# Kernel tuning notes

Measured on AMD Instinct MI355X. Metric: run time of the kernel, lower is better.

Reference implementation:

```python
import jax, jax.numpy as jnp
import numpy as np

B, S = 512, 200            # batch, max_seq_len
D = H = 512                # embedding_dim must equal hidden_dim (ht init from embedded input)
VOCAB, USERS, SKILLS, OUT = 2002, 10000, 1001, 1001


def setup_inputs() -> dict:
    key = jax.random.key(0)
    ks = jax.random.split(key, 15)
    s = 0.05
    enc_emb = jax.random.normal(ks[0], (VOCAB, D)) * s
    enc_emb = enc_emb.at[0].set(0.0)  # padding_idx=0
    P = jax.random.normal(ks[1], (USERS, H)) * s
    Q = jax.random.normal(ks[2], (SKILLS, H)) * s
    P_bias = jax.random.normal(ks[3], (USERS, 1)) * s
    Q_bias = jax.random.normal(ks[4], (SKILLS, 1)) * s
    W_ih = jax.random.normal(ks[5], (4 * H, D)) * s   # torch LSTMCell weight_ih
    W_hh = jax.random.normal(ks[6], (4 * H, H)) * s   # torch LSTMCell weight_hh
    b_ih = jax.random.normal(ks[7], (4 * H,)) * s
    b_hh = jax.random.normal(ks[8], (4 * H,)) * s
    dec_W = jax.random.normal(ks[9], (OUT, H)) * s    # nn.Linear weight
    dec_b = jax.random.normal(ks[10], (OUT,)) * s
    main_input = jax.random.randint(ks[11], (B, S), 0, VOCAB)
    target_id = jax.random.randint(ks[12], (B, 1), 0, OUT)
    user_id_sequence = jax.random.randint(ks[13], (B, S), 0, USERS)
    skill_id_sequence = jax.random.randint(ks[14], (B, S), 0, SKILLS)
    return dict(main_input=main_input, target_id=target_id,
                user_id_sequence=user_id_sequence, skill_id_sequence=skill_id_sequence,
                enc_emb=enc_emb, P=P, Q=Q, P_bias=P_bias, Q_bias=Q_bias,
                W_ih=W_ih, W_hh=W_hh, b_ih=b_ih, b_hh=b_hh, dec_W=dec_W, dec_b=dec_b)


def reference(main_input, target_id, user_id_sequence, skill_id_sequence,
              enc_emb, P, Q, P_bias, Q_bias, W_ih, W_hh, b_ih, b_hh, dec_W, dec_b):
    x = enc_emb[main_input]                                    # [B,S,D] (dropout in eval mode = identity)
    # MF extended input: sigmoid(sum(P*Q, dim=2, keepdim) + P_bias + Q_bias) -> [B,S,1]
    mf = jax.nn.sigmoid(jnp.sum(P[user_id_sequence] * Q[skill_id_sequence], axis=2, keepdims=True)
                        + P_bias[user_id_sequence] + Q_bias[skill_id_sequence])

    def step(carry, inp):
        ht, ct = carry
        xt, et = inp                                           # xt:[B,D], et:[B,1]
        ct = ct + ct * et                                      # custom gating before cell update
        gates = xt @ W_ih.T + b_ih + ht @ W_hh.T + b_hh        # [B,4H], torch gate order i,f,g,o
        i, f, g, o = jnp.split(gates, 4, axis=-1)
        ct = jax.nn.sigmoid(f) * ct + jax.nn.sigmoid(i) * jnp.tanh(g)
        ht = jax.nn.sigmoid(o) * jnp.tanh(ct)
        return (ht, ct), None

    h0 = jnp.zeros((x.shape[0], H), x.dtype)
    (ht, _), _ = jax.lax.scan(step, (h0, h0),
                              (jnp.swapaxes(x, 0, 1), jnp.swapaxes(mf, 0, 1)))
    out = ht @ dec_W.T + dec_b                                 # [B,OUT]
    out = jnp.take_along_axis(out, target_id, axis=-1)         # [B,1]
    return jax.nn.sigmoid(out)
```

## Files before the change

### kernel.cpp

```cpp
#include <hip/hip_runtime.h>

typedef __attribute__((ext_vector_type(8))) short short8;
typedef __attribute__((ext_vector_type(4))) float floatx4;
typedef unsigned int uint;
typedef unsigned short ushort;
typedef unsigned long long ull;

#define B_ 512
#define S_ 200
#define H_ 512
#define VOCAB_ 2002

__device__ __forceinline__ ushort f2bfbits(float f) {
  union { float f; uint u; } c; c.f = f;
  uint u = c.u;
  u += 0x7fffu + ((u >> 16) & 1u);
  return (ushort)(u >> 16);
}
__device__ __forceinline__ float bf2f_(ushort u) {
  union { uint i; float f; } c; c.i = ((uint)u) << 16; return c.f;
}
__device__ __forceinline__ float sigmoidf_(float x) { return 1.f / (1.f + __expf(-x)); }
__device__ __forceinline__ float tanhf_(float x) { return 2.f / (1.f + __expf(-2.f * x)) - 1.f; }
__device__ __forceinline__ float clamp30(float x) { return fminf(fmaxf(x, -30.f), 30.f); }

__device__ __forceinline__ void split8(const float* p, short8& hi, short8& lo) {
#pragma unroll
  for (int j = 0; j < 8; ++j) {
    const float f = p[j];
    const ushort h = f2bfbits(f);
    hi[j] = (short)h;
    lo[j] = (short)f2bfbits(f - bf2f_(h));
  }
}

template <typename ET>
__global__ void encg_kernel(const float* __restrict__ emb, const float* __restrict__ Wih,
                            ET* __restrict__ encg) {
  const int w = threadIdx.x >> 6, l = threadIdx.x & 63;
  const int ln = l & 15, lk = l >> 4;
  const int n = (blockIdx.x * 4 + w) * 16 + ln;
  const int m = blockIdx.y * 16 + ln;
  const int mA = (m < VOCAB_) ? m : 0;
  const float* ap = emb + (size_t)mA * 512 + lk * 8;
  const float* bp = Wih + (size_t)n * 512 + lk * 8;
  floatx4 acc = {0.f, 0.f, 0.f, 0.f};
#pragma unroll 4
  for (int kk = 0; kk < 16; ++kk) {
    short8 ah, al, bh, bl;
    split8(ap + kk * 32, ah, al);
    split8(bp + kk * 32, bh, bl);
    acc = __builtin_amdgcn_mfma_f32_16x16x32_bf16(ah, bh, acc, 0, 0, 0);
    acc = __builtin_amdgcn_mfma_f32_16x16x32_bf16(ah, bl, acc, 0, 0, 0);
    acc = __builtin_amdgcn_mfma_f32_16x16x32_bf16(al, bh, acc, 0, 0, 0);
  }
#pragma unroll
  for (int r = 0; r < 4; ++r) {
    const int mo = blockIdx.y * 16 + lk * 4 + r;
    if (mo < VOCAB_) {
      if constexpr (sizeof(ET) == 2)
        encg[(size_t)mo * 2048 + n] = (ET)f2bfbits(acc[r]);
      else
        encg[(size_t)mo * 2048 + n] = acc[r];
    }
  }
}

__global__ void mf_kernel(const int* __restrict__ us, const int* __restrict__ ss,
                          const float* __restrict__ P, const float* __restrict__ Q,
                          const float* __restrict__ Pb, const float* __restrict__ Qb,
                          float* __restrict__ etb) {
  const int s = blockIdx.x;
  const int w = threadIdx.x >> 6, l = threadIdx.x & 63;
  const int b = blockIdx.y * 4 + w;
  const int u = us[b * S_ + s];
  const int k = ss[b * S_ + s];
  const float4 p0 = *(const float4*)(P + (size_t)u * 512 + l * 8);
  const float4 p1 = *(const float4*)(P + (size_t)u * 512 + l * 8 + 4);
  const float4 q0 = *(const float4*)(Q + (size_t)k * 512 + l * 8);
  const float4 q1 = *(const float4*)(Q + (size_t)k * 512 + l * 8 + 4);
  float dot = p0.x*q0.x + p0.y*q0.y + p0.z*q0.z + p0.w*q0.w
            + p1.x*q1.x + p1.y*q1.y + p1.z*q1.z + p1.w*q1.w;
#pragma unroll
  for (int off = 32; off > 0; off >>= 1) dot += __shfl_xor(dot, off);
  if (l == 0)
    etb[s * B_ + b] = sigmoidf_(dot + Pb[u] + Qb[k]);
}

template <typename ET>
__global__ __launch_bounds__(512, 2) void lstm_kernel(
    const int* __restrict__ tok, const ET* __restrict__ encg,
    const float* __restrict__ etb, const float* __restrict__ Whh,
    const float* __restrict__ bih, const float* __restrict__ bhh,
    ushort* ht_hi, ushort* ht_lo, int* ctr) {
  __shared__ __align__(16) ushort Ah_lds[32 * 528];
  __shared__ __align__(16) ushort Al_lds[32 * 528];
  __shared__ __align__(16) float gp_lds[128 * 36];

  const int bid = blockIdx.x;
  const int g = bid & 15, ns = bid >> 4;
  const int b0 = g * 32, h0 = ns * 32;
  const int tid = threadIdx.x;
  const int w = tid >> 6, l = tid & 63;
  const int ln = l & 15, lk = l >> 4;
  const int q = w >> 1;
  const int c0 = (w & 1) * 16;

  int* const myslot = ctr + g * 256 + ns * 16;
  int* const gslots = ctr + g * 256;

  short8 Bh[16], Bl[16];
  {
    const float* wr = Whh + (size_t)(q * 512 + h0 + c0 + ln) * 512 + lk * 8;
#pragma unroll 4
    for (int kk = 0; kk < 16; ++kk)
      split8(wr + kk * 32, Bh[kk], Bl[kk]);
  }

  const int sr = tid >> 4;
  const int sc = tid & 15;
  const int hh = sc * 2;
  const int bg = b0 + sr;
  float ct0 = 0.f, ct1 = 0.f;

  float bs[4][2];
#pragma unroll
  for (int qq = 0; qq < 4; ++qq) {
    const int col = qq * 512 + h0 + hh;
    bs[qq][0] = bih[col] + bhh[col];
    bs[qq][1] = bih[col + 1] + bhh[col + 1];
  }

  for (int s = 0; s < S_; ++s) {
    const int tv = tok[bg * S_ + s];
    float ev = etb[s * B_ + bg];
    float ex[4], ey[4];
#pragma unroll
    for (int qq = 0; qq < 4; ++qq) {
      if constexpr (sizeof(ET) == 2) {
        const uint e2 = *(const uint*)((const ushort*)encg + (size_t)tv * 2048 + qq * 512 + h0 + hh);
        ex[qq] = bf2f_((ushort)(e2 & 0xffffu)); ey[qq] = bf2f_((ushort)(e2 >> 16));
      } else {
        const float2 e = *(const float2*)((const float*)encg + (size_t)tv * 2048 + qq * 512 + h0 + hh);
        ex[qq] = e.x; ey[qq] = e.y;
      }
    }

    if (s > 0) {
      if (tid < 16) {
        while (__hip_atomic_load(gslots + tid * 16, __ATOMIC_RELAXED,
                                 __HIP_MEMORY_SCOPE_AGENT) < s) {}
      }
      __syncthreads();
    }
    const size_t rdo = (size_t)(s & 1) * (B_ * H_);
    const size_t wro = (size_t)((s & 1) ^ 1) * (B_ * H_);

    {
      const size_t go = rdo + (size_t)(b0 + sr) * 512 + sc * 32;
      const int lo_ = sr * 528 + sc * 32;
#pragma unroll
      for (int i = 0; i < 8; ++i)
        *(ull*)(Ah_lds + lo_ + i * 4) =
            __hip_atomic_load((const ull*)(ht_hi + go + i * 4), __ATOMIC_RELAXED, __HIP_MEMORY_SCOPE_AGENT);
#pragma unroll
      for (int i = 0; i < 8; ++i)
        *(ull*)(Al_lds + lo_ + i * 4) =
            __hip_atomic_load((const ull*)(ht_lo + go + i * 4), __ATOMIC_RELAXED, __HIP_MEMORY_SCOPE_AGENT);
    }
    __syncthreads();

    floatx4 acc[2];
    acc[0] = (floatx4){0.f, 0.f, 0.f, 0.f};
    acc[1] = (floatx4){0.f, 0.f, 0.f, 0.f};
#pragma unroll
    for (int mt = 0; mt < 2; ++mt)
#pragma unroll
      for (int kk = 0; kk < 16; ++kk) {
        const int ao = (mt * 16 + ln) * 528 + kk * 32 + lk * 8;
        const short8 ah = *(const short8*)(Ah_lds + ao);
        const short8 al = *(const short8*)(Al_lds + ao);
        acc[mt] = __builtin_amdgcn_mfma_f32_16x16x32_bf16(ah, Bh[kk], acc[mt], 0, 0, 0);
        acc[mt] = __builtin_amdgcn_mfma_f32_16x16x32_bf16(ah, Bl[kk], acc[mt], 0, 0, 0);
        acc[mt] = __builtin_amdgcn_mfma_f32_16x16x32_bf16(al, Bh[kk], acc[mt], 0, 0, 0);
      }
#pragma unroll
    for (int mt = 0; mt < 2; ++mt)
      *(floatx4*)(gp_lds + (w * 16 + ln) * 36 + mt * 16 + lk * 4) = acc[mt];
    __syncthreads();

    {
      ev = fminf(fmaxf(ev, 0.f), 1.f);
      float Gv[4][2];
#pragma unroll
      for (int qq = 0; qq < 4; ++qq) {
        Gv[qq][0] = clamp30(gp_lds[(qq * 32 + hh) * 36 + sr] + ex[qq] + bs[qq][0]);
        Gv[qq][1] = clamp30(gp_lds[(qq * 32 + hh + 1) * 36 + sr] + ey[qq] + bs[qq][1]);
      }
      const float scale = 1.f + ev;
      float c0v = ct0 * scale;
      c0v = sigmoidf_(Gv[1][0]) * c0v + sigmoidf_(Gv[0][0]) * tanhf_(Gv[2][0]);
      const float h0v = sigmoidf_(Gv[3][0]) * tanhf_(c0v);
      ct0 = c0v;
      float c1v = ct1 * scale;
      c1v = sigmoidf_(Gv[1][1]) * c1v + sigmoidf_(Gv[0][1]) * tanhf_(Gv[2][1]);
      const float h1v = sigmoidf_(Gv[3][1]) * tanhf_(c1v);
      ct1 = c1v;
      const ushort h0h = f2bfbits(h0v), h1h = f2bfbits(h1v);
      const ushort h0l = f2bfbits(h0v - bf2f_(h0h)), h1l = f2bfbits(h1v - bf2f_(h1h));
      const size_t wo = wro + (size_t)bg * 512 + h0 + hh;
      __hip_atomic_store((uint*)(ht_hi + wo), (uint)h0h | ((uint)h1h << 16),
                         __ATOMIC_RELAXED, __HIP_MEMORY_SCOPE_AGENT);
      __hip_atomic_store((uint*)(ht_lo + wo), (uint)h0l | ((uint)h1l << 16),
                         __ATOMIC_RELAXED, __HIP_MEMORY_SCOPE_AGENT);
    }
    __syncthreads();
    if (tid == 0)
      __hip_atomic_store(myslot, s + 1, __ATOMIC_RELAXED, __HIP_MEMORY_SCOPE_AGENT);
  }
}

__global__ void dec_kernel(const ushort* __restrict__ hthi, const ushort* __restrict__ htlo,
                           const float* __restrict__ decW, const float* __restrict__ decb,
                           const int* __restrict__ tgt, float* __restrict__ out) {
  const int w = threadIdx.x >> 6, l = threadIdx.x & 63;
  const int b = blockIdx.x * 4 + w;
  const int t = tgt[b];
  const uint4 hv = *(const uint4*)(hthi + (size_t)b * 512 + l * 8);
  const uint4 lv = *(const uint4*)(htlo + (size_t)b * 512 + l * 8);
  const float4 w0 = *(const float4*)(decW + (size_t)t * 512 + l * 8);
  const float4 w1 = *(const float4*)(decW + (size_t)t * 512 + l * 8 + 4);
  const uint ha[4] = {hv.x, hv.y, hv.z, hv.w};
  const uint la[4] = {lv.x, lv.y, lv.z, lv.w};
  float hf[8];
#pragma unroll
  for (int i = 0; i < 4; ++i) {
    hf[2*i]   = bf2f_((ushort)(ha[i] & 0xffffu)) + bf2f_((ushort)(la[i] & 0xffffu));
    hf[2*i+1] = bf2f_((ushort)(ha[i] >> 16))     + bf2f_((ushort)(la[i] >> 16));
  }
  float dot = hf[0]*w0.x + hf[1]*w0.y + hf[2]*w0.z + hf[3]*w0.w
            + hf[4]*w1.x + hf[5]*w1.y + hf[6]*w1.z + hf[7]*w1.w;
#pragma unroll
  for (int off = 32; off > 0; off >>= 1) dot += __shfl_xor(dot, off);
  if (l == 0) out[b] = sigmoidf_(dot + decb[t]);
}

extern "C" void kernel_launch(void* const* d_in, const int* in_sizes, int n_in,
                              void* d_out, int out_size, void* d_ws, size_t ws_size,
                              hipStream_t stream) {
  (void)in_sizes; (void)n_in; (void)out_size;
  const int* main_input = (const int*)d_in[0];
  const int* target_id  = (const int*)d_in[1];
  const int* user_seq   = (const int*)d_in[2];
  const int* skill_seq  = (const int*)d_in[3];
  const float* enc_emb  = (const float*)d_in[4];
  const float* P        = (const float*)d_in[5];
  const float* Q        = (const float*)d_in[6];
  const float* Pb       = (const float*)d_in[7];
  const float* Qb       = (const float*)d_in[8];
  const float* W_ih     = (const float*)d_in[9];
  const float* W_hh     = (const float*)d_in[10];
  const float* b_ih     = (const float*)d_in[11];
  const float* b_hh     = (const float*)d_in[12];
  const float* dec_W    = (const float*)d_in[13];
  const float* dec_b    = (const float*)d_in[14];
  float* out = (float*)d_out;

  char* wsb = (char*)d_ws;
  ushort* ht_hi = (ushort*)wsb;
  ushort* ht_lo = (ushort*)(wsb + 1048576);
  int* ctr = (int*)(wsb + 2097152);
  float* etb = (float*)(wsb + 2113536);
  char* encb = wsb + 2523136;
  const bool enc32 = ws_size >= (size_t)2523136 + 16400384;

  hipMemsetAsync(wsb, 0, 2113536, stream);

  if (enc32)
    encg_kernel<float><<<dim3(32, 126), dim3(256), 0, stream>>>(enc_emb, W_ih, (float*)encb);
  else
    encg_kernel<ushort><<<dim3(32, 126), dim3(256), 0, stream>>>(enc_emb, W_ih, (ushort*)encb);
  mf_kernel<<<dim3(200, 128), dim3(256), 0, stream>>>(user_seq, skill_seq, P, Q, Pb, Qb, etb);
  if (enc32)
    lstm_kernel<float><<<dim3(256), dim3(512), 0, stream>>>(
        main_input, (const float*)encb, etb, W_hh, b_ih, b_hh, ht_hi, ht_lo, ctr);
  else
    lstm_kernel<ushort><<<dim3(256), dim3(512), 0, stream>>>(
        main_input, (const ushort*)encb, etb, W_hh, b_ih, b_hh, ht_hi, ht_lo, ctr);
  dec_kernel<<<dim3(128), dim3(256), 0, stream>>>(ht_hi, ht_lo, dec_W, dec_b, target_id, out);
}
```

Measured before the change: 2.997 ms.

## Co-locate batch groups per XCD and use non-atomic exchange when all peers share an XCD

Result: slower. 3.083 ms (+2.9%).

```diff
diff --git a/kernel.cpp b/kernel.cpp
--- a/kernel.cpp
+++ b/kernel.cpp
@@ -96,9 +96,12 @@
   __shared__ __align__(16) ushort Ah_lds[32 * 528];
   __shared__ __align__(16) ushort Al_lds[32 * 528];
   __shared__ __align__(16) float gp_lds[128 * 36];
+  __shared__ int cen_lds[16];
+  __shared__ int fast_flag;
 
   const int bid = blockIdx.x;
-  const int g = bid & 15, ns = bid >> 4;
+  const int g = (bid & 7) * 2 + ((bid >> 3) & 1);
+  const int ns = bid >> 4;
   const int b0 = g * 32, h0 = ns * 32;
   const int tid = threadIdx.x;
   const int w = tid >> 6, l = tid & 63;
@@ -108,6 +111,13 @@
 
   int* const myslot = ctr + g * 256 + ns * 16;
   int* const gslots = ctr + g * 256;
+  int* const census = ctr + 4096;
+
+  if (tid == 0) {
+    const int xcd = (int)__builtin_amdgcn_s_getreg(6164);
+    __hip_atomic_store(census + (g * 16 + ns) * 16, xcd + 1,
+                       __ATOMIC_RELAXED, __HIP_MEMORY_SCOPE_AGENT);
+  }
 
   short8 Bh[16], Bl[16];
   {
@@ -116,6 +126,24 @@
     for (int kk = 0; kk < 16; ++kk)
       split8(wr + kk * 32, Bh[kk], Bl[kk]);
   }
+
+  if (tid < 16) {
+    int v;
+    do {
+      v = __hip_atomic_load(census + (g * 16 + tid) * 16,
+                            __ATOMIC_RELAXED, __HIP_MEMORY_SCOPE_AGENT);
+    } while (v == 0);
+    cen_lds[tid] = v;
+  }
+  __syncthreads();
+  if (tid == 0) {
+    int f = 1;
+#pragma unroll
+    for (int i = 1; i < 16; ++i) f &= (cen_lds[i] == cen_lds[0]);
+    fast_flag = f;
+  }
+  __syncthreads();
+  const bool fastp = (fast_flag != 0);
 
   const int sr = tid >> 4;
   const int sc = tid & 15;
@@ -148,8 +176,12 @@
 
     if (s > 0) {
       if (tid < 16) {
-        while (__hip_atomic_load(gslots + tid * 16, __ATOMIC_RELAXED,
-                                 __HIP_MEMORY_SCOPE_AGENT) < s) {}
+        if (fastp) {
+          while (((volatile const int*)gslots)[tid * 16] < s) {}
+        } else {
+          while (__hip_atomic_load(gslots + tid * 16, __ATOMIC_RELAXED,
+                                   __HIP_MEMORY_SCOPE_AGENT) < s) {}
+        }
       }
       __syncthreads();
     }
@@ -159,14 +191,23 @@
     {
       const size_t go = rdo + (size_t)(b0 + sr) * 512 + sc * 32;
       const int lo_ = sr * 528 + sc * 32;
-#pragma unroll
-      for (int i = 0; i < 8; ++i)
-        *(ull*)(Ah_lds + lo_ + i * 4) =
-            __hip_atomic_load((const ull*)(ht_hi + go + i * 4), __ATOMIC_RELAXED, __HIP_MEMORY_SCOPE_AGENT);
-#pragma unroll
-      for (int i = 0; i < 8; ++i)
-        *(ull*)(Al_lds + lo_ + i * 4) =
-            __hip_atomic_load((const ull*)(ht_lo + go + i * 4), __ATOMIC_RELAXED, __HIP_MEMORY_SCOPE_AGENT);
+      if (fastp) {
+        volatile const ull* sh = (volatile const ull*)(ht_hi + go);
+        volatile const ull* sl = (volatile const ull*)(ht_lo + go);
+#pragma unroll
+        for (int i = 0; i < 8; ++i) *(ull*)(Ah_lds + lo_ + i * 4) = sh[i];
+#pragma unroll
+        for (int i = 0; i < 8; ++i) *(ull*)(Al_lds + lo_ + i * 4) = sl[i];
+      } else {
+#pragma unroll
+        for (int i = 0; i < 8; ++i)
+          *(ull*)(Ah_lds + lo_ + i * 4) =
+              __hip_atomic_load((const ull*)(ht_hi + go + i * 4), __ATOMIC_RELAXED, __HIP_MEMORY_SCOPE_AGENT);
+#pragma unroll
+        for (int i = 0; i < 8; ++i)
+          *(ull*)(Al_lds + lo_ + i * 4) =
+              __hip_atomic_load((const ull*)(ht_lo + go + i * 4), __ATOMIC_RELAXED, __HIP_MEMORY_SCOPE_AGENT);
+      }
     }
     __syncthreads();
 
@@ -209,14 +250,21 @@
       const ushort h0h = f2bfbits(h0v), h1h = f2bfbits(h1v);
       const ushort h0l = f2bfbits(h0v - bf2f_(h0h)), h1l = f2bfbits(h1v - bf2f_(h1h));
       const size_t wo = wro + (size_t)bg * 512 + h0 + hh;
-      __hip_atomic_store((uint*)(ht_hi + wo), (uint)h0h | ((uint)h1h << 16),
-                         __ATOMIC_RELAXED, __HIP_MEMORY_SCOPE_AGENT);
-      __hip_atomic_store((uint*)(ht_lo + wo), (uint)h0l | ((uint)h1l << 16),
-                         __ATOMIC_RELAXED, __HIP_MEMORY_SCOPE_AGENT);
+      const uint ph = (uint)h0h | ((uint)h1h << 16);
+      const uint pl = (uint)h0l | ((uint)h1l << 16);
+      if (fastp) {
+        *(uint*)(ht_hi + wo) = ph;
+        *(uint*)(ht_lo + wo) = pl;
+      } else {
+        __hip_atomic_store((uint*)(ht_hi + wo), ph, __ATOMIC_RELAXED, __HIP_MEMORY_SCOPE_AGENT);
+        __hip_atomic_store((uint*)(ht_lo + wo), pl, __ATOMIC_RELAXED, __HIP_MEMORY_SCOPE_AGENT);
+      }
     }
     __syncthreads();
-    if (tid == 0)
-      __hip_atomic_store(myslot, s + 1, __ATOMIC_RELAXED, __HIP_MEMORY_SCOPE_AGENT);
+    if (tid == 0) {
+      if (fastp) ((volatile int*)myslot)[0] = s + 1;
+      else __hip_atomic_store(myslot, s + 1, __ATOMIC_RELAXED, __HIP_MEMORY_SCOPE_AGENT);
+    }
   }
 }
 
@@ -270,11 +318,11 @@
   ushort* ht_hi = (ushort*)wsb;
   ushort* ht_lo = (ushort*)(wsb + 1048576);
   int* ctr = (int*)(wsb + 2097152);
-  float* etb = (float*)(wsb + 2113536);
-  char* encb = wsb + 2523136;
-  const bool enc32 = ws_size >= (size_t)2523136 + 16400384;
-
-  hipMemsetAsync(wsb, 0, 2113536, stream);
+  float* etb = (float*)(wsb + 2129920);
+  char* encb = wsb + 2539520;
+  const bool enc32 = ws_size >= (size_t)2539520 + 16400384;
+
+  hipMemsetAsync(wsb, 0, 2129920, stream);
 
   if (enc32)
     encg_kernel<float><<<dim3(32, 126), dim3(256), 0, stream>>>(enc_emb, W_ih, (float*)encb);
```
